# Performance work log

Hardware: AMD Instinct MI355X
Metric: run time of the kernel (lower is better)

Reference implementation:

```python
import jax, jax.numpy as jnp
import numpy as np

B, N_IN, N_OUT, N_NODES, N_EDGES = 64, 128, 256, 20000, 320000
ITERS, LEAK, IN_AMP, OUT_AMP = 150, 0.01, 1.2, 1.2


def setup_inputs() -> dict:
    key = jax.random.key(0)
    ks = jax.random.split(key, 8)
    x = jax.random.normal(ks[0], (B, N_IN), dtype=jnp.float32)
    # projection weights (inputAmplitude / projectionAmplitude * ones)
    in_w = IN_AMP * jnp.ones((N_IN,), dtype=jnp.float32)
    out_w = OUT_AMP * jnp.ones((N_OUT,), dtype=jnp.float32)
    rec_w = 0.1 + 0.1 * jax.random.uniform(ks[1], (N_EDGES,), dtype=jnp.float32)
    inhib = jax.random.bernoulli(ks[2], 0.3, (N_EDGES,))
    rec_w = jnp.where(inhib, -rec_w, rec_w)
    biases = 0.001 * jnp.ones((N_NODES, 1), dtype=jnp.float32)
    rows = jax.random.randint(ks[3], (N_EDGES,), 0, N_NODES)
    cols = jax.random.randint(ks[4], (N_EDGES,), 0, N_NODES)
    in_idx = jax.random.randint(ks[5], (N_IN,), 0, N_NODES)
    out_idx = jax.random.randint(ks[6], (N_OUT,), 0, N_NODES)
    return {"x": x, "in_w": in_w, "out_w": out_w, "rec_w": rec_w,
            "biases": biases, "rows": rows, "cols": cols,
            "in_idx": in_idx, "out_idx": out_idx}


def reference(x, in_w, out_w, rec_w, biases, rows, cols, in_idx, out_idx):
    n_nodes = biases.shape[0]

    def mml_act(v):
        # leaky below 0, Michaelis-Menten-like saturation above 0.5
        v = jnp.where(v < 0, v * LEAK, v)
        return jnp.where(v > 0.5, 1.0 - 0.25 / v, v)

    def spmv(h):
        # A @ h with A in COO form: out[r] += w_e * h[c]
        msg = rec_w[:, None] * h[cols]                      # [E, B]
        return jax.ops.segment_sum(msg, rows, num_segments=n_nodes)

    # input projection: scatter weighted inputs into node vector
    y = jnp.zeros((x.shape[0], n_nodes), x.dtype).at[:, in_idx].set(in_w * x)
    b_in = y.T + biases                                      # [N, B]

    def step(h, _):
        return mml_act(spmv(h) + b_in), None

    h0 = jnp.zeros_like(b_in)
    hT, _ = jax.lax.scan(step, h0, None, length=ITERS)
    xhat = hT.T                                              # [B, N]
    return out_w * xhat[:, out_idx]                          # [B, n_out]
```

## Files before the change

kernel.cpp:

```cpp
#include <hip/hip_runtime.h>
#include <hip/hip_fp16.h>

#define N_NODES 20000
#define N_EDGES 320000
#define BATCH   64
#define N_IN    128
#define N_OUT   256
#define CAP     64
#define ITERS   150
#define LEAK    0.01f

#define CNT_MASK 0x3FFFFFFF
#define FLAG_BIT (1 << 30)

#define NSLICE 32
#define BPS    8
#define NPB    2500
#define NT     1024
#define NBLK   (NSLICE * BPS)
#define SLICE_U32 20480
#define OWN_U128  625
#define PAIRS  32
#define TAG_STRIDE 32

typedef unsigned int uint;
typedef unsigned long long ull;
typedef _Float16 h2_t __attribute__((ext_vector_type(2)));
typedef uint u32x4 __attribute__((ext_vector_type(4)));

__device__ __forceinline__ void st128_mall(u32x4* p, u32x4 v) {
    asm volatile("global_store_dwordx4 %0, %1, off sc0 sc1"
                 :: "v"(p), "v"(v) : "memory");
}
__device__ __forceinline__ void st32_mall(uint* p, uint v) {
    asm volatile("global_store_dword %0, %1, off sc0 sc1"
                 :: "v"(p), "v"(v) : "memory");
}
__device__ __forceinline__ uint ld32_mall(const uint* p) {
    uint v;
    asm volatile("global_load_dword %0, %1, off sc0 sc1\n\t"
                 "s_waitcnt vmcnt(0)"
                 : "=v"(v) : "v"(p) : "memory");
    return v;
}

__device__ __forceinline__ float fdot2u(uint w, uint h, float acc) {
    union { uint u; h2_t h; } a, b; a.u = w; b.u = h;
    return __builtin_amdgcn_fdot2(a.h, b.h, acc, false);
}

__global__ void setup_kernel(uint* __restrict__ hGA, uint* __restrict__ hGB,
                             int* __restrict__ cnt,
                             uint* __restrict__ colpair, uint* __restrict__ wpair,
                             uint* __restrict__ tags) {
    int idx = blockIdx.x * blockDim.x + threadIdx.x;
    int stride = gridDim.x * blockDim.x;
    for (int i = idx; i < NSLICE * SLICE_U32; i += stride) { hGA[i] = 0u; hGB[i] = 0u; }
    for (int i = idx; i < N_NODES; i += stride) cnt[i] = 0;
    for (int i = idx; i < PAIRS * N_NODES; i += stride) { colpair[i] = 0u; wpair[i] = 0u; }
    for (int i = idx; i < NSLICE * BPS * TAG_STRIDE; i += stride) tags[i] = 0u;
}

__global__ void input_scatter_kernel(float* __restrict__ bin,
                                     const float* __restrict__ x,
                                     const float* __restrict__ in_w,
                                     const int* __restrict__ in_idx,
                                     const float* __restrict__ biases,
                                     int* __restrict__ cnt) {
    int i = blockIdx.x;
    int b = threadIdx.x;
    int node = in_idx[i];
    if (b == 0) atomicOr(&cnt[node], FLAG_BIT);
    for (int j = i + 1; j < N_IN; j++)
        if (in_idx[j] == node) return;
    bin[node * BATCH + b] = biases[node] + in_w[i] * x[b * N_IN + i];
}

__global__ void ell_build_kernel(const int* __restrict__ rows,
                                 const int* __restrict__ cols,
                                 const float* __restrict__ rec_w,
                                 uint* __restrict__ colpair, uint* __restrict__ wpair,
                                 int* __restrict__ cnt) {
    int e = blockIdx.x * blockDim.x + threadIdx.x;
    if (e >= N_EDGES) return;
    int r = rows[e];
    int s = atomicAdd(&cnt[r], 1) & CNT_MASK;
    if (s < CAP) {
        int p = s >> 1, sh = (s & 1) * 16;
        atomicOr(&colpair[(size_t)p * N_NODES + r], (uint)cols[e] << sh);
        uint hw = (uint)__half_as_ushort(__float2half(rec_w[e]));
        atomicOr(&wpair[(size_t)p * N_NODES + r], hw << sh);
    }
}

__global__ __launch_bounds__(NT) void sort_kernel(const int* __restrict__ cnt,
                                                  int* __restrict__ permG,
                                                  int* __restrict__ rankOf) {
    __shared__ int hist[65], off[65];
    int nbase = blockIdx.x * NPB;
    int tid = threadIdx.x;
    if (tid < 65) hist[tid] = 0;
    __syncthreads();
    for (int r = tid; r < NPB; r += NT) {
        int c = cnt[nbase + r] & CNT_MASK; if (c > CAP) c = CAP;
        atomicAdd(&hist[c], 1);
    }
    __syncthreads();
    if (tid == 0) {
        int run = 0;
        for (int c = CAP; c >= 0; c--) { off[c] = run; run += hist[c]; }
    }
    __syncthreads();
    for (int r = tid; r < NPB; r += NT) {
        int c = cnt[nbase + r] & CNT_MASK; if (c > CAP) c = CAP;
        int rk = atomicAdd(&off[c], 1);
        permG[nbase + rk] = nbase + r;
        rankOf[nbase + r] = nbase + rk;
    }
}

__global__ void reorder_kernel(const uint* __restrict__ colpair,
                               const uint* __restrict__ wpair,
                               const int* __restrict__ permG,
                               const int* __restrict__ rankOf,
                               uint2* __restrict__ cwR) {
    int r = blockIdx.x * blockDim.x + threadIdx.x;
    int p = blockIdx.y;
    if (r >= N_NODES) return;
    size_t o = (size_t)p * N_NODES;
    int n = permG[r];
    uint cc = colpair[o + n];
    uint lo = (uint)rankOf[cc & 0xFFFFu];
    uint hi = (uint)rankOf[cc >> 16];
    cwR[o + r] = make_uint2(lo | (hi << 16), wpair[o + n]);
}

__device__ __forceinline__ uint finish_node(float a0, float a1, float b0, float b1) {
    float r0 = b0 + a0, r1 = b1 + a1;
    float u0 = (r0 < 0.f) ? r0 * LEAK : r0;
    float u1 = (r1 < 0.f) ? r1 * LEAK : r1;
    float v0 = (u0 > 0.5f) ? (1.0f - 0.25f / u0) : u0;
    float v1 = (u1 > 0.5f) ? (1.0f - 0.25f / u1) : u1;
    union { __half2 h; uint u; } p;
    p.h = __halves2half2(__float2half(v0), __float2half(v1));
    return p.u;
}

__device__ __forceinline__ void hoist_consts(
        int nbase, int tid, int s,
        const int* __restrict__ cnt, const int* __restrict__ permG,
        const float* __restrict__ bin, const float* __restrict__ biases,
        int* rank, float* mb0, float* mb1, bool* ma, int& kp) {
    int kmax = 0;
#pragma unroll
    for (int j = 0; j < 3; j++) {
        int sl = 3 * tid + j;
        ma[j] = (sl < NPB);
        rank[j] = nbase + (ma[j] ? sl : 0);
        int n = permG[rank[j]];
        int cv = cnt[n];
        int c = cv & CNT_MASK; if (c > CAP) c = CAP;
        if (ma[j] && c > kmax) kmax = c;
        if (cv & FLAG_BIT) {
            mb0[j] = bin[(size_t)n * BATCH + 2 * s];
            mb1[j] = bin[(size_t)n * BATCH + 2 * s + 1];
        } else {
            float bb = biases[n]; mb0[j] = bb; mb1[j] = bb;
        }
    }
    kp = (kmax + 1) >> 1;
}

__device__ __forceinline__ void compute_pairs(
        const int* rank, int kp,
        const uint2* __restrict__ cwR,
        const uint* __restrict__ lds_h, float* a0, float* a1) {
    a0[0] = a0[1] = a0[2] = 0.f;
    a1[0] = a1[1] = a1[2] = 0.f;
#pragma unroll 2
    for (int p = 0; p < kp; p++) {
        size_t o = (size_t)p * N_NODES;
#pragma unroll
        for (int j = 0; j < 3; j++) {
            uint2 m = cwR[o + rank[j]];
            uint ha = lds_h[m.x & 0xFFFFu];
            uint hb = lds_h[m.x >> 16];
            uint lo = __builtin_amdgcn_perm(hb, ha, 0x05040100u);
            uint hi = __builtin_amdgcn_perm(hb, ha, 0x07060302u);
            a0[j] = fdot2u(m.y, lo, a0[j]);
            a1[j] = fdot2u(m.y, hi, a1[j]);
        }
    }
}

__global__ __launch_bounds__(NT) void persistent_kernel(
        uint* hGA, uint* hGB,
        const float* __restrict__ bin, const float* __restrict__ biases,
        const uint2* __restrict__ cwR,
        const int* __restrict__ cnt, const int* __restrict__ permG,
        uint* tags) {
    extern __shared__ uint lds_h[];
    int bid = blockIdx.x, tid = threadIdx.x;
    int s = bid >> 3, sub = bid & 7;
    int nbase = sub * NPB;
    const int wave = tid >> 6, lane = tid & 63;
    const int sb = wave >> 1, half = wave & 1;

    int rank[3]; float mb0[3], mb1[3]; bool ma[3]; int kp;
    hoist_consts(nbase, tid, s, cnt, permG, bin, biases, rank, mb0, mb1, ma, kp);

    for (int i = tid; i < SLICE_U32; i += NT) lds_h[i] = 0u;
    __syncthreads();

    uint* hA_s = hGA + (size_t)s * SLICE_U32;
    uint* hB_s = hGB + (size_t)s * SLICE_U32;
    uint* mytag = &tags[(s * BPS + sub) * TAG_STRIDE];

    for (int t = 0; t < ITERS; t++) {
        uint* hout = (t & 1) ? hB_s : hA_s;

        float a0[3], a1[3];
        compute_pairs(rank, kp, cwR, lds_h, a0, a1);
        uint v[3];
#pragma unroll
        for (int j = 0; j < 3; j++) v[j] = finish_node(a0[j], a1[j], mb0[j], mb1[j]);

        __syncthreads();
#pragma unroll
        for (int j = 0; j < 3; j++)
            if (ma[j]) lds_h[rank[j]] = v[j];
        __syncthreads();

        if (tid < OWN_U128) {
            int i = sub * OWN_U128 + tid;
            st128_mall((u32x4*)hout + i, ((const u32x4*)lds_h)[i]);
        }
        if (t == ITERS - 1) break;

        __syncthreads();
        if (tid == 0) st32_mall(mytag, (uint)(t + 1));

        if (sb != sub) {
            if (lane == 0) {
                const uint* rt = &tags[(s * BPS + sb) * TAG_STRIDE];
                while (ld32_mall(rt) < (uint)(t + 1)) __builtin_amdgcn_s_sleep(2);
            }
            const u32x4* sp = (const u32x4*)hout + sb * OWN_U128;
            u32x4* dp = (u32x4*)lds_h + sb * OWN_U128;
            int it0 = half * 64 + lane;
            int it4 = it0 + 512;
            int c4 = (it4 <= 624) ? it4 : 624;
            u32x4 r0, r1, r2, r3, r4;
            asm volatile(
                "global_load_dwordx4 %0, %5, off sc0 sc1\n\t"
                "global_load_dwordx4 %1, %6, off sc0 sc1\n\t"
                "global_load_dwordx4 %2, %7, off sc0 sc1\n\t"
                "global_load_dwordx4 %3, %8, off sc0 sc1\n\t"
                "global_load_dwordx4 %4, %9, off sc0 sc1\n\t"
                "s_waitcnt vmcnt(0)"
                : "=&v"(r0), "=&v"(r1), "=&v"(r2), "=&v"(r3), "=&v"(r4)
                : "v"(sp + it0), "v"(sp + it0 + 128), "v"(sp + it0 + 256),
                  "v"(sp + it0 + 384), "v"(sp + c4)
                : "memory");
            dp[it0] = r0; dp[it0 + 128] = r1; dp[it0 + 256] = r2;
            dp[it0 + 384] = r3;
            if (it4 <= 624) dp[it4] = r4;
        }
        __syncthreads();
    }
}

__global__ __launch_bounds__(NT) void step_kernel(
        const uint* __restrict__ hprev, uint* __restrict__ hnext,
        const float* __restrict__ bin, const float* __restrict__ biases,
        const uint2* __restrict__ cwR,
        const int* __restrict__ cnt, const int* __restrict__ permG) {
    extern __shared__ uint lds_h[];
    int bid = blockIdx.x, tid = threadIdx.x;
    int s = bid >> 3, sub = bid & 7;
    int nbase = sub * NPB;

    int rank[3]; float mb0[3], mb1[3]; bool ma[3]; int kp;
    hoist_consts(nbase, tid, s, cnt, permG, bin, biases, rank, mb0, mb1, ma, kp);

    const uint* hp = hprev + (size_t)s * SLICE_U32;
    for (int i = tid; i < SLICE_U32; i += NT) lds_h[i] = hp[i];
    __syncthreads();

    float a0[3], a1[3];
    compute_pairs(rank, kp, cwR, lds_h, a0, a1);
    uint* ho = hnext + (size_t)s * SLICE_U32;
#pragma unroll
    for (int j = 0; j < 3; j++)
        if (ma[j]) ho[rank[j]] = finish_node(a0[j], a1[j], mb0[j], mb1[j]);
}

__global__ void output_kernel(const uint* __restrict__ hfinal,
                              const int* __restrict__ out_idx,
                              const int* __restrict__ rankOf,
                              const float* __restrict__ out_w,
                              float* __restrict__ out) {
    int o = threadIdx.x;
    int b = blockIdx.x;
    uint v = hfinal[(size_t)(b >> 1) * SLICE_U32 + rankOf[out_idx[o]]];
    unsigned short h = (b & 1) ? (unsigned short)(v >> 16) : (unsigned short)(v & 0xFFFF);
    out[b * N_OUT + o] = out_w[o] * __half2float(__ushort_as_half(h));
}

extern "C" void kernel_launch(void* const* d_in, const int* in_sizes, int n_in,
                              void* d_out, int out_size, void* d_ws, size_t ws_size,
                              hipStream_t stream) {
    const float* x      = (const float*)d_in[0];
    const float* in_w   = (const float*)d_in[1];
    const float* out_w  = (const float*)d_in[2];
    const float* rec_w  = (const float*)d_in[3];
    const float* biases = (const float*)d_in[4];
    const int*   rows   = (const int*)d_in[5];
    const int*   cols   = (const int*)d_in[6];
    const int*   in_idx = (const int*)d_in[7];
    const int*   oidx   = (const int*)d_in[8];
    float* out = (float*)d_out;

    char* ws = (char*)d_ws;
    uint*  hGA     = (uint*)ws;  ws += (size_t)NSLICE * SLICE_U32 * 4;
    uint*  hGB     = (uint*)ws;  ws += (size_t)NSLICE * SLICE_U32 * 4;
    float* bin     = (float*)ws; ws += (size_t)N_NODES * BATCH * 4;
    uint*  colpair = (uint*)ws;  ws += (size_t)PAIRS * N_NODES * 4;
    uint*  wpair   = (uint*)ws;  ws += (size_t)PAIRS * N_NODES * 4;
    uint2* cwR     = (uint2*)ws; ws += (size_t)PAIRS * N_NODES * 8;
    int*   cnt     = (int*)ws;   ws += (size_t)N_NODES * 4;
    int*   permG   = (int*)ws;   ws += (size_t)N_NODES * 4;
    int*   rankOf  = (int*)ws;   ws += (size_t)N_NODES * 4;
    uint*  tags    = (uint*)ws;  ws += (size_t)NSLICE * BPS * TAG_STRIDE * 4;

    const int shmem = SLICE_U32 * 4;
    hipFuncSetAttribute((const void*)persistent_kernel,
                        hipFuncAttributeMaxDynamicSharedMemorySize, shmem);
    hipFuncSetAttribute((const void*)step_kernel,
                        hipFuncAttributeMaxDynamicSharedMemorySize, shmem);

    setup_kernel<<<2048, 256, 0, stream>>>(hGA, hGB, cnt, colpair, wpair, tags);
    input_scatter_kernel<<<N_IN, BATCH, 0, stream>>>(bin, x, in_w, in_idx,
                                                     biases, cnt);
    ell_build_kernel<<<(N_EDGES + 255) / 256, 256, 0, stream>>>(rows, cols, rec_w,
                                                                colpair, wpair, cnt);
    sort_kernel<<<N_NODES / NPB, NT, 0, stream>>>(cnt, permG, rankOf);
    reorder_kernel<<<dim3((N_NODES + 255) / 256, PAIRS), 256, 0, stream>>>(
        colpair, wpair, permG, rankOf, cwR);

    void* args[] = { (void*)&hGA, (void*)&hGB, (void*)&bin, (void*)&biases,
                     (void*)&cwR, (void*)&cnt, (void*)&permG, (void*)&tags };
    hipError_t ce = hipLaunchCooperativeKernel((void*)persistent_kernel,
                                               dim3(NBLK), dim3(NT),
                                               args, shmem, stream);
    const uint* hfinal;
    if (ce == hipSuccess) {
        hfinal = hGB;
    } else {
        uint* pa = hGA;
        uint* pb = hGB;
        for (int t = 0; t < ITERS; t++) {
            step_kernel<<<NBLK, NT, shmem, stream>>>(pa, pb, bin, biases,
                                                     cwR, cnt, permG);
            uint* tmp = pa; pa = pb; pb = tmp;
        }
        hfinal = pa;
    }

    output_kernel<<<BATCH, N_OUT, 0, stream>>>(hfinal, oidx, rankOf, out_w, out);
}
```

Measured before the change: 1.067 ms.

## Double-buffer LDS slice to drop two barriers and store results directly

The persistent kernel now keeps two LDS copies of the slice. Each thread writes its finished node values into the next buffer and also stores them straight to global memory with per-dword stores. This replaces the sync, LDS write, sync and 128-bit copy-out sequence. The peer-fetch wave mapping is redone so 14 waves cover the 7 other sub-blocks, and the buffers swap each iteration. LDS use per block doubles to 160 KB, and the scattered 32-bit global stores replace coalesced 128-bit ones.

```diff
diff --git a/kernel.cpp b/kernel.cpp
--- a/kernel.cpp
+++ b/kernel.cpp
@@ -28,10 +28,6 @@
 typedef _Float16 h2_t __attribute__((ext_vector_type(2)));
 typedef uint u32x4 __attribute__((ext_vector_type(4)));
 
-__device__ __forceinline__ void st128_mall(u32x4* p, u32x4 v) {
-    asm volatile("global_store_dwordx4 %0, %1, off sc0 sc1"
-                 :: "v"(p), "v"(v) : "memory");
-}
 __device__ __forceinline__ void st32_mall(uint* p, uint v) {
     asm volatile("global_store_dword %0, %1, off sc0 sc1"
                  :: "v"(p), "v"(v) : "memory");
@@ -199,54 +195,55 @@
         const uint2* __restrict__ cwR,
         const int* __restrict__ cnt, const int* __restrict__ permG,
         uint* tags) {
-    extern __shared__ uint lds_h[];
+    extern __shared__ uint lds_all[];
+    uint* bufA = lds_all;
+    uint* bufB = lds_all + SLICE_U32;
     int bid = blockIdx.x, tid = threadIdx.x;
     int s = bid >> 3, sub = bid & 7;
     int nbase = sub * NPB;
     const int wave = tid >> 6, lane = tid & 63;
-    const int sb = wave >> 1, half = wave & 1;
 
     int rank[3]; float mb0[3], mb1[3]; bool ma[3]; int kp;
     hoist_consts(nbase, tid, s, cnt, permG, bin, biases, rank, mb0, mb1, ma, kp);
 
-    for (int i = tid; i < SLICE_U32; i += NT) lds_h[i] = 0u;
+    for (int i = tid; i < SLICE_U32; i += NT) bufA[i] = 0u;
     __syncthreads();
 
     uint* hA_s = hGA + (size_t)s * SLICE_U32;
     uint* hB_s = hGB + (size_t)s * SLICE_U32;
     uint* mytag = &tags[(s * BPS + sub) * TAG_STRIDE];
 
+    uint* cur = bufA;
+    uint* nxt = bufB;
+
     for (int t = 0; t < ITERS; t++) {
         uint* hout = (t & 1) ? hB_s : hA_s;
 
         float a0[3], a1[3];
-        compute_pairs(rank, kp, cwR, lds_h, a0, a1);
-        uint v[3];
+        compute_pairs(rank, kp, cwR, cur, a0, a1);
 #pragma unroll
-        for (int j = 0; j < 3; j++) v[j] = finish_node(a0[j], a1[j], mb0[j], mb1[j]);
-
-        __syncthreads();
-#pragma unroll
-        for (int j = 0; j < 3; j++)
-            if (ma[j]) lds_h[rank[j]] = v[j];
-        __syncthreads();
-
-        if (tid < OWN_U128) {
-            int i = sub * OWN_U128 + tid;
-            st128_mall((u32x4*)hout + i, ((const u32x4*)lds_h)[i]);
+        for (int j = 0; j < 3; j++) {
+            if (ma[j]) {
+                uint v = finish_node(a0[j], a1[j], mb0[j], mb1[j]);
+                nxt[rank[j]] = v;
+                st32_mall(&hout[rank[j]], v);
+            }
         }
         if (t == ITERS - 1) break;
 
         __syncthreads();
         if (tid == 0) st32_mall(mytag, (uint)(t + 1));
 
-        if (sb != sub) {
+        if (wave < 14) {
+            int sb_idx = wave >> 1;
+            int sb = sb_idx + (sb_idx >= sub ? 1 : 0);
+            int half = wave & 1;
             if (lane == 0) {
                 const uint* rt = &tags[(s * BPS + sb) * TAG_STRIDE];
                 while (ld32_mall(rt) < (uint)(t + 1)) __builtin_amdgcn_s_sleep(2);
             }
             const u32x4* sp = (const u32x4*)hout + sb * OWN_U128;
-            u32x4* dp = (u32x4*)lds_h + sb * OWN_U128;
+            u32x4* dp = (u32x4*)nxt + sb * OWN_U128;
             int it0 = half * 64 + lane;
             int it4 = it0 + 512;
             int c4 = (it4 <= 624) ? it4 : 624;
@@ -267,6 +264,7 @@
             if (it4 <= 624) dp[it4] = r4;
         }
         __syncthreads();
+        uint* tmp = cur; cur = nxt; nxt = tmp;
     }
 }
 
@@ -333,11 +331,12 @@
     int*   rankOf  = (int*)ws;   ws += (size_t)N_NODES * 4;
     uint*  tags    = (uint*)ws;  ws += (size_t)NSLICE * BPS * TAG_STRIDE * 4;
 
-    const int shmem = SLICE_U32 * 4;
+    const int shmem_p = 2 * SLICE_U32 * 4;
+    const int shmem_f = SLICE_U32 * 4;
     hipFuncSetAttribute((const void*)persistent_kernel,
-                        hipFuncAttributeMaxDynamicSharedMemorySize, shmem);
+                        hipFuncAttributeMaxDynamicSharedMemorySize, shmem_p);
     hipFuncSetAttribute((const void*)step_kernel,
-                        hipFuncAttributeMaxDynamicSharedMemorySize, shmem);
+                        hipFuncAttributeMaxDynamicSharedMemorySize, shmem_f);
 
     setup_kernel<<<2048, 256, 0, stream>>>(hGA, hGB, cnt, colpair, wpair, tags);
     input_scatter_kernel<<<N_IN, BATCH, 0, stream>>>(bin, x, in_w, in_idx,
@@ -352,7 +351,7 @@
                      (void*)&cwR, (void*)&cnt, (void*)&permG, (void*)&tags };
     hipError_t ce = hipLaunchCooperativeKernel((void*)persistent_kernel,
                                                dim3(NBLK), dim3(NT),
-                                               args, shmem, stream);
+                                               args, shmem_p, stream);
     const uint* hfinal;
     if (ce == hipSuccess) {
         hfinal = hGB;
@@ -360,8 +359,8 @@
         uint* pa = hGA;
         uint* pb = hGB;
         for (int t = 0; t < ITERS; t++) {
-            step_kernel<<<NBLK, NT, shmem, stream>>>(pa, pb, bin, biases,
-                                                     cwR, cnt, permG);
+            step_kernel<<<NBLK, NT, shmem_f, stream>>>(pa, pb, bin, biases,
+                                                       cwR, cnt, permG);
             uint* tmp = pa; pa = pb; pb = tmp;
         }
         hfinal = pa;
```

Result: slower. 1.209 ms (+13.3%).
